# Kernel tuning notes

Hardware: AMD Instinct MI355X
Metric: run time of the kernel (lower is better)

The kernel has to match this reference:

```python
import jax, jax.numpy as jnp
import numpy as np

NUM_EXPERTS = 64
GROUP_SIZE = 4
NUM_GROUPS = NUM_EXPERTS // GROUP_SIZE  # 16
TOP_K = 2
B, S, D = 8, 4096, 2048


def setup_inputs() -> dict:
    key = jax.random.key(0)
    k1, k2, k3 = jax.random.split(key, 3)
    x = jax.random.normal(k1, (B, S, D), dtype=jnp.float32)
    # nn.Linear weight layout [out, in], init std=0.001
    Wg = jax.random.normal(k2, (NUM_GROUPS, D), dtype=jnp.float32) * 0.001
    We = jax.random.normal(k3, (GROUP_SIZE, D), dtype=jnp.float32) * 0.001
    return {"x": x, "Wg": Wg, "We": We}


def reference(x, Wg, We):
    b, s, d = x.shape
    n_tok = b * s
    x_flat = x.reshape(n_tok, d)

    # Stage 1: group routing (top-1 group)
    group_logits = x_flat @ Wg.T                      # [N, G]
    group_probs = jax.nn.softmax(group_logits, axis=-1)
    top_gw, top_gi = jax.lax.top_k(group_probs, 1)    # [N, 1]
    chosen_group = top_gi[:, 0]                        # [N] int
    chosen_group_w = top_gw[:, 0]                      # [N]

    # Stage 2: local expert routing (top-k within group)
    local_logits = x_flat @ We.T                       # [N, group_size]
    local_probs = jax.nn.softmax(local_logits, axis=-1)
    expert_offset = chosen_group * GROUP_SIZE          # [N]
    top_lw, top_li = jax.lax.top_k(local_probs, TOP_K) # [N, k]
    top_expert_idx = expert_offset[:, None] + top_li   # [N, k]

    top_lw = top_lw / (jnp.sum(top_lw, axis=-1, keepdims=True) + 1e-7)
    final_weights = chosen_group_w[:, None] * top_lw   # [N, k]

    # Dispatch mask: scatter final_weights at chosen expert columns.
    # top-k local indices are distinct, so set (== torch scatter_) is safe.
    rows = jnp.arange(n_tok)[:, None]
    dispatch_mask = jnp.zeros((n_tok, NUM_EXPERTS), dtype=x.dtype)
    dispatch_mask = dispatch_mask.at[rows, top_expert_idx].set(final_weights)

    # Auxiliary losses
    expert_load = dispatch_mask.sum(axis=0)            # [E]
    target_load = expert_load.sum() / NUM_EXPERTS
    load_balance_loss = jnp.mean((expert_load - target_load) ** 2)
    z_loss = jnp.mean(group_logits ** 2) + jnp.mean(local_logits ** 2)
    router_loss = 0.001 * (load_balance_loss + z_loss)

    return jax.lax.stop_gradient(final_weights), dispatch_mask, router_loss
```

## Files before the change

### kernel.cpp

```cpp
#include <hip/hip_runtime.h>


#define NTOK    32768
#define DIM     2048
#define NG      16
#define GS      4
#define NE      64
#define NR      20
#define DC      256
#define NCHUNK  (DIM / DC)
#define TPB     256
#define TPW     4
#define TPBK    16
#define NSHADOW 32

__global__ __launch_bounds__(TPB, 2) void router_main(
    const float* __restrict__ x,
    const float* __restrict__ Wg,
    const float* __restrict__ We,
    float* __restrict__ fw_out,
    float* __restrict__ dm_out,
    float* __restrict__ ws)
{
    __shared__ float wlds[NR * DC];
    __shared__ float lds_load[NE];
    __shared__ float lds_z;

    const int tid  = threadIdx.x;
    const int lane = tid & 63;
    const int wave = tid >> 6;
    const long t_base = (long)blockIdx.x * TPBK + wave * TPW;

    if (tid < NE) lds_load[tid] = 0.0f;
    if (tid == 0) lds_z = 0.0f;

    float acc[TPW][NR];
    #pragma unroll
    for (int t = 0; t < TPW; ++t)
        #pragma unroll
        for (int r = 0; r < NR; ++r) acc[t][r] = 0.0f;

    for (int c = 0; c < NCHUNK; ++c) {
        __syncthreads();
        #pragma unroll
        for (int k = 0; k < (NR * DC) / (TPB * 4); ++k) {
            int f   = (k * TPB + tid) * 4;
            int r   = f >> 8;
            int col = f & (DC - 1);
            const float* src = (r < NG) ? (Wg + (size_t)r * DIM)
                                        : (We + (size_t)(r - NG) * DIM);
            *(float4*)(&wlds[r * DC + col]) = *(const float4*)(src + c * DC + col);
        }
        __syncthreads();

        float4 xa[TPW];
        #pragma unroll
        for (int t = 0; t < TPW; ++t) {
            const float4* xp = (const float4*)(x + (size_t)(t_base + t) * DIM + c * DC);
            xa[t] = xp[lane];
        }
        #pragma unroll
        for (int r = 0; r < NR; ++r) {
            float4 w = *(const float4*)(&wlds[r * DC + lane * 4]);
            #pragma unroll
            for (int t = 0; t < TPW; ++t) {
                acc[t][r] += xa[t].x * w.x + xa[t].y * w.y
                           + xa[t].z * w.z + xa[t].w * w.w;
            }
        }
    }

    #pragma unroll
    for (int t = 0; t < TPW; ++t)
        #pragma unroll
        for (int r = 0; r < NR; ++r) {
            float v = acc[t][r];
            #pragma unroll
            for (int s = 32; s > 0; s >>= 1) v += __shfl_xor(v, s, 64);
            acc[t][r] = v;
        }

    #pragma unroll
    for (int t = 0; t < TPW; ++t) {
        float m16 = acc[t][0];
        #pragma unroll
        for (int r = 1; r < NG; ++r) m16 = fmaxf(m16, acc[t][r]);
        float den = 0.0f, bm = -1.0f; int gi = 0;
        #pragma unroll
        for (int r = 0; r < NG; ++r) {
            float e = expf(acc[t][r] - m16);
            den += e;
            if (e > bm) { bm = e; gi = r; }
        }
        float gw = bm / den;

        float m4 = fmaxf(fmaxf(acc[t][NG + 0], acc[t][NG + 1]),
                         fmaxf(acc[t][NG + 2], acc[t][NG + 3]));
        float pr[GS]; float s4 = 0.0f;
        #pragma unroll
        for (int r = 0; r < GS; ++r) { pr[r] = expf(acc[t][NG + r] - m4); s4 += pr[r]; }
        float inv4 = 1.0f / s4;
        #pragma unroll
        for (int r = 0; r < GS; ++r) pr[r] *= inv4;

        int i0 = 0; float v0 = pr[0];
        #pragma unroll
        for (int r = 1; r < GS; ++r) if (pr[r] > v0) { v0 = pr[r]; i0 = r; }
        int i1 = -1; float v1 = -1.0f;
        #pragma unroll
        for (int r = 0; r < GS; ++r) if (r != i0 && pr[r] > v1) { v1 = pr[r]; i1 = r; }

        float nrm = v0 + v1 + 1e-7f;
        float sf0 = gw * (v0 / nrm);
        float sf1 = gw * (v1 / nrm);
        int   se0 = (gi << 2) + i0;
        int   se1 = (gi << 2) + i1;

        float sg = 0.0f;
        #pragma unroll
        for (int r = 0; r < NG; ++r) sg += acc[t][r] * acc[t][r];
        float sl = 0.0f;
        #pragma unroll
        for (int r = 0; r < GS; ++r) sl += acc[t][NG + r] * acc[t][NG + r];
        float sz = sg * (1.0f / 16.0f) + sl * 0.25f;

        const long tok = t_base + t;
        if (lane < 16) {
            int col4 = lane * 4;
            float4 v;
            v.x = (col4 + 0 == se0) ? sf0 : (col4 + 0 == se1) ? sf1 : 0.0f;
            v.y = (col4 + 1 == se0) ? sf0 : (col4 + 1 == se1) ? sf1 : 0.0f;
            v.z = (col4 + 2 == se0) ? sf0 : (col4 + 2 == se1) ? sf1 : 0.0f;
            v.w = (col4 + 3 == se0) ? sf0 : (col4 + 3 == se1) ? sf1 : 0.0f;
            *(float4*)(dm_out + (size_t)tok * NE + col4) = v;
        } else if (lane == 16) {
            *(float2*)(fw_out + tok * 2) = make_float2(sf0, sf1);
        } else if (lane == 17) {
            atomicAdd(&lds_load[se0], sf0);
        } else if (lane == 18) {
            atomicAdd(&lds_load[se1], sf1);
        } else if (lane == 19) {
            atomicAdd(&lds_z, sz);
        }
    }

    __syncthreads();
    if (tid < NE) atomicAdd(&ws[(blockIdx.x & (NSHADOW - 1)) * NE + tid], lds_load[tid]);
    if (tid == 0) atomicAdd(&ws[NSHADOW * NE], lds_z);
}

__global__ void router_finalize(const float* __restrict__ ws, float* __restrict__ out_loss)
{
    int e = threadIdx.x;
    float load = 0.0f;
    #pragma unroll
    for (int s = 0; s < NSHADOW; ++s) load += ws[s * NE + e];
    float tot = load;
    #pragma unroll
    for (int s = 32; s > 0; s >>= 1) tot += __shfl_xor(tot, s, 64);
    float target = tot * (1.0f / NE);
    float dev = load - target;
    float sq = dev * dev;
    #pragma unroll
    for (int s = 32; s > 0; s >>= 1) sq += __shfl_xor(sq, s, 64);
    if (e == 0) {
        float lb = sq * (1.0f / NE);
        float z  = ws[NSHADOW * NE] * (1.0f / NTOK);
        out_loss[0] = 0.001f * (lb + z);
    }
}

extern "C" void kernel_launch(void* const* d_in, const int* in_sizes, int n_in,
                              void* d_out, int out_size, void* d_ws, size_t ws_size,
                              hipStream_t stream)
{
    const float* x  = (const float*)d_in[0];
    const float* Wg = (const float*)d_in[1];
    const float* We = (const float*)d_in[2];
    float* out = (float*)d_out;
    float* fw  = out;
    float* dm  = out + (size_t)NTOK * 2;
    float* ls  = out + (size_t)NTOK * 2 + (size_t)NTOK * NE;
    float* ws  = (float*)d_ws;

    hipMemsetAsync(ws, 0, (NSHADOW * NE + 1) * sizeof(float), stream);
    router_main<<<NTOK / TPBK, TPB, 0, stream>>>(x, Wg, We, fw, dm, ws);
    router_finalize<<<1, 64, 0, stream>>>(ws, ls);
}
```

Before: 408.1 us.

## Drop LDS weight staging, double-buffer x loads with nontemporal hints

Removes the shared-memory staging of router weights and the two block barriers per chunk. Each wave now reads the 20 weight rows directly from global memory, relying on cache. Activation chunks are prefetched one chunk ahead into registers using nontemporal loads, so streaming x overlaps the FMA work. This adds register pressure and repeated global weight reads per wave in exchange for no barrier stalls.

```diff
diff --git a/kernel.cpp b/kernel.cpp
--- a/kernel.cpp
+++ b/kernel.cpp
@@ -14,6 +14,12 @@
 #define TPBK    16
 #define NSHADOW 32
 
+typedef float f4 __attribute__((ext_vector_type(4)));
+
+__device__ __forceinline__ f4 ldnt(const float* p) {
+    return __builtin_nontemporal_load((const f4*)p);
+}
+
 __global__ __launch_bounds__(TPB, 2) void router_main(
     const float* __restrict__ x,
     const float* __restrict__ Wg,
@@ -22,7 +28,6 @@
     float* __restrict__ dm_out,
     float* __restrict__ ws)
 {
-    __shared__ float wlds[NR * DC];
     __shared__ float lds_load[NE];
     __shared__ float lds_z;
 
@@ -33,6 +38,7 @@
 
     if (tid < NE) lds_load[tid] = 0.0f;
     if (tid == 0) lds_z = 0.0f;
+    __syncthreads();
 
     float acc[TPW][NR];
     #pragma unroll
@@ -40,32 +46,44 @@
         #pragma unroll
         for (int r = 0; r < NR; ++r) acc[t][r] = 0.0f;
 
-    for (int c = 0; c < NCHUNK; ++c) {
-        __syncthreads();
-        #pragma unroll
-        for (int k = 0; k < (NR * DC) / (TPB * 4); ++k) {
-            int f   = (k * TPB + tid) * 4;
-            int r   = f >> 8;
-            int col = f & (DC - 1);
-            const float* src = (r < NG) ? (Wg + (size_t)r * DIM)
-                                        : (We + (size_t)(r - NG) * DIM);
-            *(float4*)(&wlds[r * DC + col]) = *(const float4*)(src + c * DC + col);
-        }
-        __syncthreads();
-
-        float4 xa[TPW];
-        #pragma unroll
-        for (int t = 0; t < TPW; ++t) {
-            const float4* xp = (const float4*)(x + (size_t)(t_base + t) * DIM + c * DC);
-            xa[t] = xp[lane];
-        }
+    f4 xa[TPW], xb[TPW];
+    #pragma unroll
+    for (int t = 0; t < TPW; ++t)
+        xa[t] = ldnt(x + (size_t)(t_base + t) * DIM + lane * 4);
+
+    #pragma unroll 1
+    for (int c = 0; c < NCHUNK; c += 2) {
+        #pragma unroll
+        for (int t = 0; t < TPW; ++t)
+            xb[t] = ldnt(x + (size_t)(t_base + t) * DIM + (c + 1) * DC + lane * 4);
+
         #pragma unroll
         for (int r = 0; r < NR; ++r) {
-            float4 w = *(const float4*)(&wlds[r * DC + lane * 4]);
+            const float* wp = (r < NG) ? (Wg + (size_t)r * DIM)
+                                       : (We + (size_t)(r - NG) * DIM);
+            f4 w = *(const f4*)(wp + c * DC + lane * 4);
             #pragma unroll
             for (int t = 0; t < TPW; ++t) {
                 acc[t][r] += xa[t].x * w.x + xa[t].y * w.y
                            + xa[t].z * w.z + xa[t].w * w.w;
+            }
+        }
+
+        if (c + 2 < NCHUNK) {
+            #pragma unroll
+            for (int t = 0; t < TPW; ++t)
+                xa[t] = ldnt(x + (size_t)(t_base + t) * DIM + (c + 2) * DC + lane * 4);
+        }
+
+        #pragma unroll
+        for (int r = 0; r < NR; ++r) {
+            const float* wp = (r < NG) ? (Wg + (size_t)r * DIM)
+                                       : (We + (size_t)(r - NG) * DIM);
+            f4 w = *(const f4*)(wp + (c + 1) * DC + lane * 4);
+            #pragma unroll
+            for (int t = 0; t < TPW; ++t) {
+                acc[t][r] += xb[t].x * w.x + xb[t].y * w.y
+                           + xb[t].z * w.z + xb[t].w * w.w;
             }
         }
     }
```

Result: slower. 429.3 us (+5.2%).

## Double-buffer x chunks via global_load_lds and read weights directly from L2

Applied to the files above, without the earlier changes.

Replaces the per-chunk LDS staging of the router weights with direct global loads of Wg/We, which are small and cache-resident. The token activations are instead prefetched one chunk ahead into a double-buffered LDS area using the async global_load_lds builtin, so the next chunk's load overlaps the current chunk's math. Launch bounds are raised to four blocks per SM to increase occupancy. This risks extra register pressure and per-wave weight reads from cache, and it relies on the async LDS load having completed by the barrier at the end of each iteration without an explicit wait.

```diff
diff --git a/kernel.cpp b/kernel.cpp
--- a/kernel.cpp
+++ b/kernel.cpp
@@ -14,7 +14,16 @@
 #define TPBK    16
 #define NSHADOW 32
 
-__global__ __launch_bounds__(TPB, 2) void router_main(
+typedef float f4 __attribute__((ext_vector_type(4)));
+
+__device__ __forceinline__ void gl_lds16(const float* g, float* l) {
+    __builtin_amdgcn_global_load_lds(
+        (const __attribute__((address_space(1))) void*)g,
+        (__attribute__((address_space(3))) void*)l,
+        16, 0, 0);
+}
+
+__global__ __launch_bounds__(TPB, 4) void router_main(
     const float* __restrict__ x,
     const float* __restrict__ Wg,
     const float* __restrict__ We,
@@ -22,14 +31,15 @@
     float* __restrict__ dm_out,
     float* __restrict__ ws)
 {
-    __shared__ float wlds[NR * DC];
+    __shared__ float xbuf[2][TPBK * DC];
     __shared__ float lds_load[NE];
     __shared__ float lds_z;
 
     const int tid  = threadIdx.x;
     const int lane = tid & 63;
     const int wave = tid >> 6;
-    const long t_base = (long)blockIdx.x * TPBK + wave * TPW;
+    const long blk0   = (long)blockIdx.x * TPBK;
+    const long t_base = blk0 + wave * TPW;
 
     if (tid < NE) lds_load[tid] = 0.0f;
     if (tid == 0) lds_z = 0.0f;
@@ -40,34 +50,43 @@
         #pragma unroll
         for (int r = 0; r < NR; ++r) acc[t][r] = 0.0f;
 
+    #pragma unroll
+    for (int k = 0; k < TPW; ++k) {
+        const int s = wave * TPW + k;
+        gl_lds16(x + (size_t)(blk0 + s) * DIM + lane * 4, &xbuf[0][s * DC]);
+    }
+    __syncthreads();
+
+    #pragma unroll 1
     for (int c = 0; c < NCHUNK; ++c) {
-        __syncthreads();
-        #pragma unroll
-        for (int k = 0; k < (NR * DC) / (TPB * 4); ++k) {
-            int f   = (k * TPB + tid) * 4;
-            int r   = f >> 8;
-            int col = f & (DC - 1);
-            const float* src = (r < NG) ? (Wg + (size_t)r * DIM)
-                                        : (We + (size_t)(r - NG) * DIM);
-            *(float4*)(&wlds[r * DC + col]) = *(const float4*)(src + c * DC + col);
-        }
-        __syncthreads();
-
-        float4 xa[TPW];
-        #pragma unroll
-        for (int t = 0; t < TPW; ++t) {
-            const float4* xp = (const float4*)(x + (size_t)(t_base + t) * DIM + c * DC);
-            xa[t] = xp[lane];
-        }
+        if (c + 1 < NCHUNK) {
+            #pragma unroll
+            for (int k = 0; k < TPW; ++k) {
+                const int s = wave * TPW + k;
+                gl_lds16(x + (size_t)(blk0 + s) * DIM + (c + 1) * DC + lane * 4,
+                         &xbuf[(c + 1) & 1][s * DC]);
+            }
+        }
+
+        const float* xb = &xbuf[c & 1][0];
+        f4 xa[TPW];
+        #pragma unroll
+        for (int t = 0; t < TPW; ++t)
+            xa[t] = *(const f4*)(xb + (wave * TPW + t) * DC + lane * 4);
+
         #pragma unroll
         for (int r = 0; r < NR; ++r) {
-            float4 w = *(const float4*)(&wlds[r * DC + lane * 4]);
+            const float* wp = (r < NG) ? (Wg + (size_t)r * DIM)
+                                       : (We + (size_t)(r - NG) * DIM);
+            f4 w = *(const f4*)(wp + c * DC + lane * 4);
             #pragma unroll
             for (int t = 0; t < TPW; ++t) {
                 acc[t][r] += xa[t].x * w.x + xa[t].y * w.y
                            + xa[t].z * w.z + xa[t].w * w.w;
             }
         }
+
+        __syncthreads();
     }
 
     #pragma unroll
```

Result: slower. 473.3 us (+16.0%).

## Preload full Wg into LDS, stream We from registers, double-buffer x loads

Applied to the files above, without the earlier changes.

The whole group-gate weight matrix is loaded once per block into LDS with direct global-to-LDS loads, so the per-chunk barriers and restaging disappear. The four local-expert rows are read straight from global memory into registers. x and We chunks are software-pipelined with two register buffers so loads overlap the dot-product work. Blocks grow to 512 threads, and each wave handles four groups of four tokens to amortise the weight staging. The cost is a 128KB LDS footprint with more register pressure, which may limit occupancy, and nontemporal loads for x.

```diff
diff --git a/kernel.cpp b/kernel.cpp
--- a/kernel.cpp
+++ b/kernel.cpp
@@ -9,10 +9,51 @@
 #define NR      20
 #define DC      256
 #define NCHUNK  (DIM / DC)
-#define TPB     256
+#define TPB     512
 #define TPW     4
-#define TPBK    16
+#define NGRP    4
+#define TOKW    (TPW * NGRP)
+#define TPBK    (TOKW * (TPB/64))
 #define NSHADOW 32
+
+typedef float f4 __attribute__((ext_vector_type(4)));
+
+__device__ __forceinline__ f4 ldnt(const float* p) {
+    return __builtin_nontemporal_load((const f4*)p);
+}
+
+__device__ __forceinline__ void gl_lds16(const float* g, float* l) {
+    __builtin_amdgcn_global_load_lds(
+        (const __attribute__((address_space(1))) void*)g,
+        (__attribute__((address_space(3))) void*)l,
+        16, 0, 0);
+}
+
+#define PF_X(DST, G, C) { _Pragma("unroll")                                   \
+    for (int t_ = 0; t_ < TPW; ++t_)                                          \
+        DST[t_] = ldnt(xw + (size_t)((G) * TPW + t_) * DIM + (C) * DC); }
+
+#define PF_W(DST, C) { _Pragma("unroll")                                      \
+    for (int r_ = 0; r_ < GS; ++r_)                                           \
+        DST[r_] = *(const f4*)(wel + (size_t)r_ * DIM + (C) * DC); }
+
+#define COMP(C, XV, WV) {                                                     \
+    _Pragma("unroll")                                                         \
+    for (int r_ = 0; r_ < NG; ++r_) {                                         \
+        f4 w_ = *(const f4*)(wlds + r_ * DIM + (C) * DC + lane4);             \
+        _Pragma("unroll")                                                     \
+        for (int t_ = 0; t_ < TPW; ++t_)                                      \
+            acc[t_][r_] += XV[t_].x * w_.x + XV[t_].y * w_.y                  \
+                         + XV[t_].z * w_.z + XV[t_].w * w_.w;                 \
+    }                                                                         \
+    _Pragma("unroll")                                                         \
+    for (int r_ = 0; r_ < GS; ++r_) {                                         \
+        f4 w_ = WV[r_];                                                       \
+        _Pragma("unroll")                                                     \
+        for (int t_ = 0; t_ < TPW; ++t_)                                      \
+            acc[t_][NG + r_] += XV[t_].x * w_.x + XV[t_].y * w_.y             \
+                              + XV[t_].z * w_.z + XV[t_].w * w_.w;            \
+    } }
 
 __global__ __launch_bounds__(TPB, 2) void router_main(
     const float* __restrict__ x,
@@ -22,125 +63,124 @@
     float* __restrict__ dm_out,
     float* __restrict__ ws)
 {
-    __shared__ float wlds[NR * DC];
+    __shared__ float wlds[NG * DIM];
     __shared__ float lds_load[NE];
     __shared__ float lds_z;
 
-    const int tid  = threadIdx.x;
-    const int lane = tid & 63;
-    const int wave = tid >> 6;
-    const long t_base = (long)blockIdx.x * TPBK + wave * TPW;
+    const int tid   = threadIdx.x;
+    const int lane  = tid & 63;
+    const int wave  = tid >> 6;
+    const int lane4 = lane * 4;
 
     if (tid < NE) lds_load[tid] = 0.0f;
     if (tid == 0) lds_z = 0.0f;
 
+    const long twave = (long)blockIdx.x * TPBK + wave * TOKW;
+    const float* xw  = x  + (size_t)twave * DIM + lane4;
+    const float* wel = We + lane4;
+
+    #pragma unroll
+    for (int k = 0; k < 16; ++k) {
+        const int seg = wave * 16 + k;
+        gl_lds16(Wg + (size_t)seg * DC + lane4, wlds + seg * DC);
+    }
+
+    f4 xa[TPW], xb[TPW], wea[GS], web[GS];
+    PF_X(xa, 0, 0);
+    PF_W(wea, 0);
+    __syncthreads();
+
     float acc[TPW][NR];
-    #pragma unroll
-    for (int t = 0; t < TPW; ++t)
+    #pragma unroll 1
+    for (int g = 0; g < NGRP; ++g) {
         #pragma unroll
-        for (int r = 0; r < NR; ++r) acc[t][r] = 0.0f;
-
-    for (int c = 0; c < NCHUNK; ++c) {
-        __syncthreads();
+        for (int t = 0; t < TPW; ++t)
+            #pragma unroll
+            for (int r = 0; r < NR; ++r) acc[t][r] = 0.0f;
+
+        PF_X(xb, g, 1);  PF_W(web, 1);  COMP(0, xa, wea);
+        PF_X(xa, g, 2);  PF_W(wea, 2);  COMP(1, xb, web);
+        PF_X(xb, g, 3);  PF_W(web, 3);  COMP(2, xa, wea);
+        PF_X(xa, g, 4);  PF_W(wea, 4);  COMP(3, xb, web);
+        PF_X(xb, g, 5);  PF_W(web, 5);  COMP(4, xa, wea);
+        PF_X(xa, g, 6);  PF_W(wea, 6);  COMP(5, xb, web);
+        PF_X(xb, g, 7);  PF_W(web, 7);  COMP(6, xa, wea);
+        if (g + 1 < NGRP) { PF_X(xa, g + 1, 0); }
+        PF_W(wea, 0);
+        COMP(7, xb, web);
+
         #pragma unroll
-        for (int k = 0; k < (NR * DC) / (TPB * 4); ++k) {
-            int f   = (k * TPB + tid) * 4;
-            int r   = f >> 8;
-            int col = f & (DC - 1);
-            const float* src = (r < NG) ? (Wg + (size_t)r * DIM)
-                                        : (We + (size_t)(r - NG) * DIM);
-            *(float4*)(&wlds[r * DC + col]) = *(const float4*)(src + c * DC + col);
-        }
-        __syncthreads();
-
-        float4 xa[TPW];
+        for (int t = 0; t < TPW; ++t)
+            #pragma unroll
+            for (int r = 0; r < NR; ++r) {
+                float v = acc[t][r];
+                #pragma unroll
+                for (int s = 32; s > 0; s >>= 1) v += __shfl_xor(v, s, 64);
+                acc[t][r] = v;
+            }
+
         #pragma unroll
         for (int t = 0; t < TPW; ++t) {
-            const float4* xp = (const float4*)(x + (size_t)(t_base + t) * DIM + c * DC);
-            xa[t] = xp[lane];
-        }
-        #pragma unroll
-        for (int r = 0; r < NR; ++r) {
-            float4 w = *(const float4*)(&wlds[r * DC + lane * 4]);
-            #pragma unroll
-            for (int t = 0; t < TPW; ++t) {
-                acc[t][r] += xa[t].x * w.x + xa[t].y * w.y
-                           + xa[t].z * w.z + xa[t].w * w.w;
+            float m16 = acc[t][0];
+            #pragma unroll
+            for (int r = 1; r < NG; ++r) m16 = fmaxf(m16, acc[t][r]);
+            float den = 0.0f, bm = -1.0f; int gi = 0;
+            #pragma unroll
+            for (int r = 0; r < NG; ++r) {
+                float e = expf(acc[t][r] - m16);
+                den += e;
+                if (e > bm) { bm = e; gi = r; }
             }
-        }
-    }
-
-    #pragma unroll
-    for (int t = 0; t < TPW; ++t)
-        #pragma unroll
-        for (int r = 0; r < NR; ++r) {
-            float v = acc[t][r];
-            #pragma unroll
-            for (int s = 32; s > 0; s >>= 1) v += __shfl_xor(v, s, 64);
-            acc[t][r] = v;
-        }
-
-    #pragma unroll
-    for (int t = 0; t < TPW; ++t) {
-        float m16 = acc[t][0];
-        #pragma unroll
-        for (int r = 1; r < NG; ++r) m16 = fmaxf(m16, acc[t][r]);
-        float den = 0.0f, bm = -1.0f; int gi = 0;
-        #pragma unroll
-        for (int r = 0; r < NG; ++r) {
-            float e = expf(acc[t][r] - m16);
-            den += e;
-            if (e > bm) { bm = e; gi = r; }
-        }
-        float gw = bm / den;
-
-        float m4 = fmaxf(fmaxf(acc[t][NG + 0], acc[t][NG + 1]),
-                         fmaxf(acc[t][NG + 2], acc[t][NG + 3]));
-        float pr[GS]; float s4 = 0.0f;
-        #pragma unroll
-        for (int r = 0; r < GS; ++r) { pr[r] = expf(acc[t][NG + r] - m4); s4 += pr[r]; }
-        float inv4 = 1.0f / s4;
-        #pragma unroll
-        for (int r = 0; r < GS; ++r) pr[r] *= inv4;
-
-        int i0 = 0; float v0 = pr[0];
-        #pragma unroll
-        for (int r = 1; r < GS; ++r) if (pr[r] > v0) { v0 = pr[r]; i0 = r; }
-        int i1 = -1; float v1 = -1.0f;
-        #pragma unroll
-        for (int r = 0; r < GS; ++r) if (r != i0 && pr[r] > v1) { v1 = pr[r]; i1 = r; }
-
-        float nrm = v0 + v1 + 1e-7f;
-        float sf0 = gw * (v0 / nrm);
-        float sf1 = gw * (v1 / nrm);
-        int   se0 = (gi << 2) + i0;
-        int   se1 = (gi << 2) + i1;
-
-        float sg = 0.0f;
-        #pragma unroll
-        for (int r = 0; r < NG; ++r) sg += acc[t][r] * acc[t][r];
-        float sl = 0.0f;
-        #pragma unroll
-        for (int r = 0; r < GS; ++r) sl += acc[t][NG + r] * acc[t][NG + r];
-        float sz = sg * (1.0f / 16.0f) + sl * 0.25f;
-
-        const long tok = t_base + t;
-        if (lane < 16) {
-            int col4 = lane * 4;
-            float4 v;
-            v.x = (col4 + 0 == se0) ? sf0 : (col4 + 0 == se1) ? sf1 : 0.0f;
-            v.y = (col4 + 1 == se0) ? sf0 : (col4 + 1 == se1) ? sf1 : 0.0f;
-            v.z = (col4 + 2 == se0) ? sf0 : (col4 + 2 == se1) ? sf1 : 0.0f;
-            v.w = (col4 + 3 == se0) ? sf0 : (col4 + 3 == se1) ? sf1 : 0.0f;
-            *(float4*)(dm_out + (size_t)tok * NE + col4) = v;
-        } else if (lane == 16) {
-            *(float2*)(fw_out + tok * 2) = make_float2(sf0, sf1);
-        } else if (lane == 17) {
-            atomicAdd(&lds_load[se0], sf0);
-        } else if (lane == 18) {
-            atomicAdd(&lds_load[se1], sf1);
-        } else if (lane == 19) {
-            atomicAdd(&lds_z, sz);
+            float gw = bm / den;
+
+            float m4 = fmaxf(fmaxf(acc[t][NG + 0], acc[t][NG + 1]),
+                             fmaxf(acc[t][NG + 2], acc[t][NG + 3]));
+            float pr[GS]; float s4 = 0.0f;
+            #pragma unroll
+            for (int r = 0; r < GS; ++r) { pr[r] = expf(acc[t][NG + r] - m4); s4 += pr[r]; }
+            float inv4 = 1.0f / s4;
+            #pragma unroll
+            for (int r = 0; r < GS; ++r) pr[r] *= inv4;
+
+            int i0 = 0; float v0 = pr[0];
+            #pragma unroll
+            for (int r = 1; r < GS; ++r) if (pr[r] > v0) { v0 = pr[r]; i0 = r; }
+            int i1 = -1; float v1 = -1.0f;
+            #pragma unroll
+            for (int r = 0; r < GS; ++r) if (r != i0 && pr[r] > v1) { v1 = pr[r]; i1 = r; }
+
+            float nrm = v0 + v1 + 1e-7f;
+            float sf0 = gw * (v0 / nrm);
+            float sf1 = gw * (v1 / nrm);
+            int   se0 = (gi << 2) + i0;
+            int   se1 = (gi << 2) + i1;
+
+            float sg = 0.0f;
+            #pragma unroll
+            for (int r = 0; r < NG; ++r) sg += acc[t][r] * acc[t][r];
+            float sl = 0.0f;
+            #pragma unroll
+            for (int r = 0; r < GS; ++r) sl += acc[t][NG + r] * acc[t][NG + r];
+            float sz = sg * (1.0f / 16.0f) + sl * 0.25f;
+
+            const long tok = twave + g * TPW + t;
+            if (lane < 16) {
+                int col4 = lane * 4;
+                float4 v;
+                v.x = (col4 + 0 == se0) ? sf0 : (col4 + 0 == se1) ? sf1 : 0.0f;
+                v.y = (col4 + 1 == se0) ? sf0 : (col4 + 1 == se1) ? sf1 : 0.0f;
+                v.z = (col4 + 2 == se0) ? sf0 : (col4 + 2 == se1) ? sf1 : 0.0f;
+                v.w = (col4 + 3 == se0) ? sf0 : (col4 + 3 == se1) ? sf1 : 0.0f;
+                *(float4*)(dm_out + (size_t)tok * NE + col4) = v;
+            } else if (lane == 16) {
+                *(float2*)(fw_out + tok * 2) = make_float2(sf0, sf1);
+            } else if (lane == 17) {
+                atomicAdd(&lds_load[se0], sf0);
+            } else if (lane == 18) {
+                atomicAdd(&lds_load[se1], sf1);
+            } else if (lane == 19) {
+                atomicAdd(&lds_z, sz);
+            }
         }
     }
 
```

Measured after the change: 825.7 us. 102% more time.
